# Kernel tuning notes

Measured on AMD Instinct MI355X. Metric: run time of the kernel, lower is better.

Reference implementation:

```python
import jax, jax.numpy as jnp
import numpy as np

EPS = 1e-12  # matches torch F.normalize default eps behavior for l2 norm

def l2norm(t):
    # normalize along last dim, like F.normalize(t, dim=-1)
    n = jnp.sqrt(jnp.sum(t * t, axis=-1, keepdims=True))
    return t / jnp.maximum(n, EPS)

def setup_inputs() -> dict:
    key = jax.random.key(0)
    k1, k2 = jax.random.split(key)
    x = jax.random.normal(k1, (4, 4096, 256), dtype=jnp.float32)
    embeddings = l2norm(jax.random.normal(k2, (8192, 256), dtype=jnp.float32))
    return {"x": x, "embeddings": embeddings}

def reference(x, embeddings):
    """Eval-mode forward of CosineSimilarityCodebook: returns (quantized, indices)."""
    shape = x.shape
    d = shape[-1]
    flatten = l2norm(x.reshape(-1, d))          # [N, d]
    emb_n = l2norm(embeddings)                  # [K, d]
    dist = flatten @ emb_n.T                    # [N, K] cosine similarity
    indices = jnp.argmax(dist, axis=-1)         # [N]
    indices = indices.reshape(shape[:-1])       # [...]
    quantized = embeddings[indices]             # gather from UN-normalized codebook
    return quantized, indices
```

## Files before the change

### kernel.cpp

```cpp
#include <hip/hip_runtime.h>
#include <stdint.h>


#define M_ROWS 16384
#define KCODES 8192
#define DDIM   256

#define BR   128
#define BCC  128
#define BK   32
#define NSPLIT 8
#define CPS  (KCODES / NSPLIT)
#define NSLICE ((CPS / BCC) * (DDIM / BK))
#define LSCALE     512.0f
#define INV_LSCALE (1.0f / 512.0f)
#define TILE_H 4096

typedef _Float16 half8v __attribute__((ext_vector_type(8)));
typedef float    f32x4  __attribute__((ext_vector_type(4)));

__device__ __forceinline__ unsigned int fkey(float f) {
    unsigned int u = __float_as_uint(f);
    return (u & 0x80000000u) ? ~u : (u | 0x80000000u);
}

__device__ __forceinline__ void gload16(const void* g, void* l) {
    __builtin_amdgcn_global_load_lds(
        (const __attribute__((address_space(1))) void*)g,
        (__attribute__((address_space(3))) void*)l, 16, 0, 0);
}


__global__ void norm_emb_kernel(const float* __restrict__ emb, float* __restrict__ inv_norm) {
    int row  = blockIdx.x * 4 + (threadIdx.x >> 6);
    int lane = threadIdx.x & 63;
    float4 v = reinterpret_cast<const float4*>(emb + row * DDIM)[lane];
    float s = v.x * v.x + v.y * v.y + v.z * v.z + v.w * v.w;
    #pragma unroll
    for (int m = 32; m; m >>= 1) s += __shfl_xor(s, m, 64);
    if (lane == 0) inv_norm[row] = 1.0f / fmaxf(sqrtf(s), 1e-12f);
}

__global__ void split_x_kernel(const float* __restrict__ x,
                               _Float16* __restrict__ xh, _Float16* __restrict__ xl) {
    int i = (blockIdx.x * 256 + threadIdx.x) * 8;
    float4 v0 = *reinterpret_cast<const float4*>(x + i);
    float4 v1 = *reinterpret_cast<const float4*>(x + i + 4);
    float v[8] = {v0.x, v0.y, v0.z, v0.w, v1.x, v1.y, v1.z, v1.w};
    half8v h, lo;
    #pragma unroll
    for (int j = 0; j < 8; ++j) {
        _Float16 hh = (_Float16)v[j];
        h[j]  = hh;
        lo[j] = (_Float16)((v[j] - (float)hh) * LSCALE);
    }
    *reinterpret_cast<half8v*>(xh + i) = h;
    *reinterpret_cast<half8v*>(xl + i) = lo;
}

__global__ void split_e_kernel(const float* __restrict__ emb, const float* __restrict__ invn,
                               _Float16* __restrict__ eh, _Float16* __restrict__ el) {
    int i = (blockIdx.x * 256 + threadIdx.x) * 8;
    float s = invn[i >> 8];
    float4 v0 = *reinterpret_cast<const float4*>(emb + i);
    float4 v1 = *reinterpret_cast<const float4*>(emb + i + 4);
    float v[8] = {v0.x * s, v0.y * s, v0.z * s, v0.w * s,
                  v1.x * s, v1.y * s, v1.z * s, v1.w * s};
    half8v h, lo;
    #pragma unroll
    for (int j = 0; j < 8; ++j) {
        _Float16 hh = (_Float16)v[j];
        h[j]  = hh;
        lo[j] = (_Float16)((v[j] - (float)hh) * LSCALE);
    }
    *reinterpret_cast<half8v*>(eh + i) = h;
    *reinterpret_cast<half8v*>(el + i) = lo;
}


__global__ __launch_bounds__(256, 2)
void mfma3_kernel(const _Float16* __restrict__ xh, const _Float16* __restrict__ xl,
                  const _Float16* __restrict__ eh, const _Float16* __restrict__ el,
                  unsigned long long* __restrict__ best) {
    __shared__ _Float16 lds[2][4 * TILE_H];

    const int t  = threadIdx.x;
    const int l  = t & 63;
    const int w  = t >> 6;
    const int wy = w >> 1, wx = w & 1;
    const int rb = blockIdx.x * BR;
    const int cs = blockIdx.y * CPS;
    const int lr = l & 15;
    const int kg = l >> 4;

    const int s_row = l >> 2;
    const int s_kg  = (l & 3) ^ ((l >> 3) & 3);

    const int rd_off = lr * 32 + (kg ^ ((lr >> 1) & 3)) * 8;
    const int a_base = wy * 64 * 32 + rd_off;
    const int b_base = wx * 64 * 32 + rd_off;

    const _Float16* gsrc = (w == 0) ? xh : (w == 1) ? xl : (w == 2) ? eh : el;
    const int g_is_x = (w < 2);

    float bestv[16];
    unsigned int bestc[16];
    #pragma unroll
    for (int i = 0; i < 16; ++i) { bestv[i] = -1e30f; bestc[i] = 0; }

    f32x4 acc[4][4];
    f32x4 acc2[4][4];

    {
        const _Float16* gp = gsrc + (g_is_x ? rb : cs) * DDIM + s_row * DDIM + s_kg * 8;
        _Float16* lp = &lds[0][w * TILE_H];
        #pragma unroll
        for (int c = 0; c < 8; ++c)
            gload16(gp + c * 16 * DDIM, lp + c * 512);
    }
    __syncthreads();

    int buf = 0;
    #pragma unroll 1
    for (int st = 0; st < NSLICE; ++st) {
        const int cb = cs + (st >> 3) * BCC;

        if ((st & 7) == 0) {
            #pragma unroll
            for (int m = 0; m < 4; ++m)
                #pragma unroll
                for (int n = 0; n < 4; ++n) {
                    acc[m][n]  = (f32x4){0.f, 0.f, 0.f, 0.f};
                    acc2[m][n] = (f32x4){0.f, 0.f, 0.f, 0.f};
                }
        }

        if (st + 1 < NSLICE) {
            const int ncb = cs + ((st + 1) >> 3) * BCC;
            const int ndb = ((st + 1) & 7) * BK;
            const _Float16* gp = gsrc + (g_is_x ? rb : ncb) * DDIM + ndb
                                 + s_row * DDIM + s_kg * 8;
            _Float16* lp = &lds[buf ^ 1][w * TILE_H];
            #pragma unroll
            for (int c = 0; c < 8; ++c)
                gload16(gp + c * 16 * DDIM, lp + c * 512);
        }

        const _Float16* L = lds[buf];
        half8v ah[4], al[4];
        #pragma unroll
        for (int m = 0; m < 4; ++m) {
            ah[m] = *reinterpret_cast<const half8v*>(&L[0 * TILE_H + a_base + m * 512]);
            al[m] = *reinterpret_cast<const half8v*>(&L[1 * TILE_H + a_base + m * 512]);
        }
        #pragma unroll
        for (int n = 0; n < 4; ++n) {
            half8v bh = *reinterpret_cast<const half8v*>(&L[2 * TILE_H + b_base + n * 512]);
            half8v bl = *reinterpret_cast<const half8v*>(&L[3 * TILE_H + b_base + n * 512]);
            #pragma unroll
            for (int m = 0; m < 4; ++m) {
                acc[m][n]  = __builtin_amdgcn_mfma_f32_16x16x32_f16(ah[m], bh, acc[m][n],  0, 0, 0);
                acc2[m][n] = __builtin_amdgcn_mfma_f32_16x16x32_f16(ah[m], bl, acc2[m][n], 0, 0, 0);
                acc2[m][n] = __builtin_amdgcn_mfma_f32_16x16x32_f16(al[m], bh, acc2[m][n], 0, 0, 0);
            }
        }

        if ((st & 7) == 7) {
            #pragma unroll
            for (int m = 0; m < 4; ++m)
                #pragma unroll
                for (int r = 0; r < 4; ++r) {
                    int bi = m * 4 + r;
                    #pragma unroll
                    for (int n = 0; n < 4; ++n) {
                        float v = acc[m][n][r] + acc2[m][n][r] * INV_LSCALE;
                        unsigned int code = cb + wx * 64 + n * 16 + lr;
                        if (v > bestv[bi]) { bestv[bi] = v; bestc[bi] = code; }
                    }
                }
        }

        __syncthreads();
        buf ^= 1;
    }

    #pragma unroll
    for (int mb = 1; mb < 16; mb <<= 1) {
        #pragma unroll
        for (int i = 0; i < 16; ++i) {
            float ov        = __shfl_xor(bestv[i], mb, 64);
            unsigned int oc = __shfl_xor(bestc[i], mb, 64);
            if (ov > bestv[i] || (ov == bestv[i] && oc < bestc[i])) {
                bestv[i] = ov; bestc[i] = oc;
            }
        }
    }
    if (lr == 0) {
        #pragma unroll
        for (int m = 0; m < 4; ++m)
            #pragma unroll
            for (int r = 0; r < 4; ++r) {
                int row_global = rb + wy * 64 + m * 16 + (l >> 4) * 4 + r;
                int bi = m * 4 + r;
                unsigned long long key =
                    ((unsigned long long)fkey(bestv[bi]) << 32) |
                    (unsigned long long)(0xFFFFFFFFu - bestc[bi]);
                atomicMax(&best[row_global], key);
            }
    }
}

#define LDP  (BK + 8)

typedef _Float16 half4v __attribute__((ext_vector_type(4)));

__device__ __forceinline__ void split4(float a, float b, float c, float d,
                                       half4v& h, half4v& lo) {
    h[0] = (_Float16)a; lo[0] = (_Float16)((a - (float)h[0]) * LSCALE);
    h[1] = (_Float16)b; lo[1] = (_Float16)((b - (float)h[1]) * LSCALE);
    h[2] = (_Float16)c; lo[2] = (_Float16)((c - (float)h[2]) * LSCALE);
    h[3] = (_Float16)d; lo[3] = (_Float16)((d - (float)h[3]) * LSCALE);
}

__global__ __launch_bounds__(256, 2)
void mfma_argmax_fb(const float* __restrict__ x, const float* __restrict__ emb,
                    const float* __restrict__ invn, unsigned long long* __restrict__ best) {
    __shared__ _Float16 Ah[BR][LDP];
    __shared__ _Float16 Al[BR][LDP];
    __shared__ _Float16 Bh[BCC][LDP];
    __shared__ _Float16 Bl[BCC][LDP];
    const int t = threadIdx.x, l = t & 63, wid = t >> 6;
    const int wy = wid >> 1, wx = wid & 1;
    const int rb = blockIdx.x * BR, cs = blockIdx.y * CPS;
    const int lr = l & 15, lk = (l >> 4) * 8;
    const int srow = t >> 3, sc4 = (t & 7) * 4;
    float bestv[16]; unsigned int bestc[16];
    #pragma unroll
    for (int i = 0; i < 16; ++i) { bestv[i] = -1e30f; bestc[i] = 0; }
    #pragma unroll 1
    for (int cc = 0; cc < CPS; cc += BCC) {
        const int cb = cs + cc;
        float bn[4];
        #pragma unroll
        for (int it = 0; it < 4; ++it) bn[it] = invn[cb + srow + it * 32];
        f32x4 acc[4][4], acc2[4][4];
        #pragma unroll
        for (int m = 0; m < 4; ++m)
            #pragma unroll
            for (int n = 0; n < 4; ++n) {
                acc[m][n] = (f32x4){0.f,0.f,0.f,0.f}; acc2[m][n] = (f32x4){0.f,0.f,0.f,0.f};
            }
        #pragma unroll 1
        for (int db = 0; db < DDIM; db += BK) {
            __syncthreads();
            #pragma unroll
            for (int it = 0; it < 4; ++it) {
                int row = srow + it * 32;
                float4 av = *reinterpret_cast<const float4*>(x + (size_t)(rb + row) * DDIM + db + sc4);
                half4v h, lo;
                split4(av.x, av.y, av.z, av.w, h, lo);
                *reinterpret_cast<half4v*>(&Ah[row][sc4]) = h;
                *reinterpret_cast<half4v*>(&Al[row][sc4]) = lo;
                float4 bv = *reinterpret_cast<const float4*>(emb + (size_t)(cb + row) * DDIM + db + sc4);
                float s = bn[it];
                split4(bv.x * s, bv.y * s, bv.z * s, bv.w * s, h, lo);
                *reinterpret_cast<half4v*>(&Bh[row][sc4]) = h;
                *reinterpret_cast<half4v*>(&Bl[row][sc4]) = lo;
            }
            __syncthreads();
            half8v ah[4], al[4];
            #pragma unroll
            for (int m = 0; m < 4; ++m) {
                ah[m] = *reinterpret_cast<const half8v*>(&Ah[wy * 64 + m * 16 + lr][lk]);
                al[m] = *reinterpret_cast<const half8v*>(&Al[wy * 64 + m * 16 + lr][lk]);
            }
            #pragma unroll
            for (int n = 0; n < 4; ++n) {
                half8v bh = *reinterpret_cast<const half8v*>(&Bh[wx * 64 + n * 16 + lr][lk]);
                half8v bl = *reinterpret_cast<const half8v*>(&Bl[wx * 64 + n * 16 + lr][lk]);
                #pragma unroll
                for (int m = 0; m < 4; ++m) {
                    acc[m][n]  = __builtin_amdgcn_mfma_f32_16x16x32_f16(ah[m], bh, acc[m][n],  0, 0, 0);
                    acc2[m][n] = __builtin_amdgcn_mfma_f32_16x16x32_f16(ah[m], bl, acc2[m][n], 0, 0, 0);
                    acc2[m][n] = __builtin_amdgcn_mfma_f32_16x16x32_f16(al[m], bh, acc2[m][n], 0, 0, 0);
                }
            }
        }
        #pragma unroll
        for (int m = 0; m < 4; ++m)
            #pragma unroll
            for (int r = 0; r < 4; ++r) {
                int bi = m * 4 + r;
                #pragma unroll
                for (int n = 0; n < 4; ++n) {
                    float v = acc[m][n][r] + acc2[m][n][r] * INV_LSCALE;
                    unsigned int code = cb + wx * 64 + n * 16 + lr;
                    if (v > bestv[bi]) { bestv[bi] = v; bestc[bi] = code; }
                }
            }
    }
    #pragma unroll
    for (int mb = 1; mb < 16; mb <<= 1) {
        #pragma unroll
        for (int i = 0; i < 16; ++i) {
            float ov = __shfl_xor(bestv[i], mb, 64);
            unsigned int oc = __shfl_xor(bestc[i], mb, 64);
            if (ov > bestv[i] || (ov == bestv[i] && oc < bestc[i])) { bestv[i] = ov; bestc[i] = oc; }
        }
    }
    if (lr == 0) {
        #pragma unroll
        for (int m = 0; m < 4; ++m)
            #pragma unroll
            for (int r = 0; r < 4; ++r) {
                int row_global = rb + wy * 64 + m * 16 + (l >> 4) * 4 + r;
                int bi = m * 4 + r;
                unsigned long long key = ((unsigned long long)fkey(bestv[bi]) << 32) |
                                         (unsigned long long)(0xFFFFFFFFu - bestc[bi]);
                atomicMax(&best[row_global], key);
            }
    }
}

__global__ void finalize_kernel(const unsigned long long* __restrict__ best,
                                const float* __restrict__ emb,
                                float* __restrict__ out) {
    int row = blockIdx.x;
    unsigned long long b = best[row];
    unsigned int code = 0xFFFFFFFFu - (unsigned int)(b & 0xFFFFFFFFull);
    out[(size_t)row * DDIM + threadIdx.x] = emb[(size_t)code * DDIM + threadIdx.x];
    if (threadIdx.x == 0) out[(size_t)M_ROWS * DDIM + row] = (float)code;
}

extern "C" void kernel_launch(void* const* d_in, const int* in_sizes, int n_in,
                              void* d_out, int out_size, void* d_ws, size_t ws_size,
                              hipStream_t stream) {
    const float* x   = (const float*)d_in[0];
    const float* emb = (const float*)d_in[1];
    float* out = (float*)d_out;

    unsigned long long* best = (unsigned long long*)d_ws;
    float* inv_norm = (float*)((char*)d_ws + 128 * 1024);
    const size_t split_off = 160 * 1024;
    const size_t need = split_off +
                        (size_t)M_ROWS * DDIM * 2 * sizeof(_Float16) +
                        (size_t)KCODES * DDIM * 2 * sizeof(_Float16);

    hipMemsetAsync(best, 0, M_ROWS * sizeof(unsigned long long), stream);
    norm_emb_kernel<<<KCODES / 4, 256, 0, stream>>>(emb, inv_norm);

    if (ws_size >= need) {
        _Float16* xh = (_Float16*)((char*)d_ws + split_off);
        _Float16* xl = xh + (size_t)M_ROWS * DDIM;
        _Float16* eh = xl + (size_t)M_ROWS * DDIM;
        _Float16* el = eh + (size_t)KCODES * DDIM;
        split_x_kernel<<<M_ROWS * DDIM / (256 * 8), 256, 0, stream>>>(x, xh, xl);
        split_e_kernel<<<KCODES * DDIM / (256 * 8), 256, 0, stream>>>(emb, inv_norm, eh, el);
        mfma3_kernel<<<dim3(M_ROWS / BR, NSPLIT), 256, 0, stream>>>(xh, xl, eh, el, best);
    } else {
        mfma_argmax_fb<<<dim3(M_ROWS / BR, NSPLIT), 256, 0, stream>>>(x, emb, inv_norm, best);
    }
    finalize_kernel<<<M_ROWS, 256, 0, stream>>>(best, emb, out);
}
```

Baseline: 289.9 us.

## Load A fragments directly from global, stage only codebook in LDS with 8 waves

```diff
diff --git a/kernel.cpp b/kernel.cpp
--- a/kernel.cpp
+++ b/kernel.cpp
@@ -14,8 +14,8 @@
 #define NSLICE ((CPS / BCC) * (DDIM / BK))
 #define LSCALE     512.0f
 #define INV_LSCALE (1.0f / 512.0f)
-#define TILE_H 4096
-
+
+typedef _Float16 half4v __attribute__((ext_vector_type(4)));
 typedef _Float16 half8v __attribute__((ext_vector_type(8)));
 typedef float    f32x4  __attribute__((ext_vector_type(4)));
 
@@ -31,10 +31,32 @@
 }
 
 
+__global__ void norm_split_e_kernel(const float* __restrict__ emb, float* __restrict__ inv_norm,
+                                    _Float16* __restrict__ eh, _Float16* __restrict__ el) {
+    int row  = blockIdx.x * 4 + (threadIdx.x >> 6);
+    int lane = threadIdx.x & 63;
+    float4 v = reinterpret_cast<const float4*>(emb + (size_t)row * DDIM)[lane];
+    float s = v.x * v.x + v.y * v.y + v.z * v.z + v.w * v.w;
+    #pragma unroll
+    for (int m = 32; m; m >>= 1) s += __shfl_xor(s, m, 64);
+    float inv = 1.0f / fmaxf(sqrtf(s), 1e-12f);
+    if (lane == 0) inv_norm[row] = inv;
+    float sv[4] = {v.x * inv, v.y * inv, v.z * inv, v.w * inv};
+    half4v h, lo;
+    #pragma unroll
+    for (int j = 0; j < 4; ++j) {
+        _Float16 hh = (_Float16)sv[j];
+        h[j]  = hh;
+        lo[j] = (_Float16)((sv[j] - (float)hh) * LSCALE);
+    }
+    *reinterpret_cast<half4v*>(eh + (size_t)row * DDIM + lane * 4) = h;
+    *reinterpret_cast<half4v*>(el + (size_t)row * DDIM + lane * 4) = lo;
+}
+
 __global__ void norm_emb_kernel(const float* __restrict__ emb, float* __restrict__ inv_norm) {
     int row  = blockIdx.x * 4 + (threadIdx.x >> 6);
     int lane = threadIdx.x & 63;
-    float4 v = reinterpret_cast<const float4*>(emb + row * DDIM)[lane];
+    float4 v = reinterpret_cast<const float4*>(emb + (size_t)row * DDIM)[lane];
     float s = v.x * v.x + v.y * v.y + v.z * v.z + v.w * v.w;
     #pragma unroll
     for (int m = 32; m; m >>= 1) s += __shfl_xor(s, m, 64);
@@ -58,65 +80,48 @@
     *reinterpret_cast<half8v*>(xl + i) = lo;
 }
 
-__global__ void split_e_kernel(const float* __restrict__ emb, const float* __restrict__ invn,
-                               _Float16* __restrict__ eh, _Float16* __restrict__ el) {
-    int i = (blockIdx.x * 256 + threadIdx.x) * 8;
-    float s = invn[i >> 8];
-    float4 v0 = *reinterpret_cast<const float4*>(emb + i);
-    float4 v1 = *reinterpret_cast<const float4*>(emb + i + 4);
-    float v[8] = {v0.x * s, v0.y * s, v0.z * s, v0.w * s,
-                  v1.x * s, v1.y * s, v1.z * s, v1.w * s};
-    half8v h, lo;
-    #pragma unroll
-    for (int j = 0; j < 8; ++j) {
-        _Float16 hh = (_Float16)v[j];
-        h[j]  = hh;
-        lo[j] = (_Float16)((v[j] - (float)hh) * LSCALE);
-    }
-    *reinterpret_cast<half8v*>(eh + i) = h;
-    *reinterpret_cast<half8v*>(el + i) = lo;
-}
-
-
-__global__ __launch_bounds__(256, 2)
-void mfma3_kernel(const _Float16* __restrict__ xh, const _Float16* __restrict__ xl,
-                  const _Float16* __restrict__ eh, const _Float16* __restrict__ el,
-                  unsigned long long* __restrict__ best) {
-    __shared__ _Float16 lds[2][4 * TILE_H];
+
+__global__ __launch_bounds__(512, 4)
+void mfma3g_kernel(const _Float16* __restrict__ xh, const _Float16* __restrict__ xl,
+                   const _Float16* __restrict__ eh, const _Float16* __restrict__ el,
+                   unsigned long long* __restrict__ best) {
+    __shared__ _Float16 lds[2][2][4096];
 
     const int t  = threadIdx.x;
     const int l  = t & 63;
     const int w  = t >> 6;
-    const int wy = w >> 1, wx = w & 1;
+    const int wy = w >> 1;
+    const int wx = w & 1;
     const int rb = blockIdx.x * BR;
     const int cs = blockIdx.y * CPS;
     const int lr = l & 15;
     const int kg = l >> 4;
 
-    const int s_row = l >> 2;
-    const int s_kg  = (l & 3) ^ ((l >> 3) & 3);
-
-    const int rd_off = lr * 32 + (kg ^ ((lr >> 1) & 3)) * 8;
-    const int a_base = wy * 64 * 32 + rd_off;
-    const int b_base = wx * 64 * 32 + rd_off;
-
-    const _Float16* gsrc = (w == 0) ? xh : (w == 1) ? xl : (w == 2) ? eh : el;
-    const int g_is_x = (w < 2);
-
-    float bestv[16];
-    unsigned int bestc[16];
-    #pragma unroll
-    for (int i = 0; i < 16; ++i) { bestv[i] = -1e30f; bestc[i] = 0; }
-
-    f32x4 acc[4][4];
-    f32x4 acc2[4][4];
+    const int s_code  = l >> 2;
+    const int s_kslot = (l & 3) ^ ((l >> 3) & 3);
+
+    const int b_off = (wx * 64 + lr) * 32 + (kg ^ ((lr >> 1) & 3)) * 8;
+
+    const size_t ar0 = (size_t)(rb + wy * 32 + lr) * DDIM + kg * 8;
+    const size_t ar1 = (size_t)(rb + wy * 32 + 16 + lr) * DDIM + kg * 8;
+    const _Float16* pah0 = xh + ar0;
+    const _Float16* pah1 = xh + ar1;
+    const _Float16* pal0 = xl + ar0;
+    const _Float16* pal1 = xl + ar1;
+
+    float bestv[8];
+    unsigned int bestc[8];
+    #pragma unroll
+    for (int i = 0; i < 8; ++i) { bestv[i] = -1e30f; bestc[i] = 0; }
+
+    f32x4 acc[2][4];
+    f32x4 acc2[2][4];
 
     {
-        const _Float16* gp = gsrc + (g_is_x ? rb : cs) * DDIM + s_row * DDIM + s_kg * 8;
-        _Float16* lp = &lds[0][w * TILE_H];
-        #pragma unroll
-        for (int c = 0; c < 8; ++c)
-            gload16(gp + c * 16 * DDIM, lp + c * 512);
+        const _Float16* gph = eh + (size_t)(cs + w * 16 + s_code) * DDIM + s_kslot * 8;
+        const _Float16* gpl = el + (size_t)(cs + w * 16 + s_code) * DDIM + s_kslot * 8;
+        gload16(gph, &lds[0][0][w * 512]);
+        gload16(gpl, &lds[0][1][w * 512]);
     }
     __syncthreads();
 
@@ -124,10 +129,11 @@
     #pragma unroll 1
     for (int st = 0; st < NSLICE; ++st) {
         const int cb = cs + (st >> 3) * BCC;
+        const int db = (st & 7) * BK;
 
         if ((st & 7) == 0) {
             #pragma unroll
-            for (int m = 0; m < 4; ++m)
+            for (int m = 0; m < 2; ++m)
                 #pragma unroll
                 for (int n = 0; n < 4; ++n) {
                     acc[m][n]  = (f32x4){0.f, 0.f, 0.f, 0.f};
@@ -138,36 +144,33 @@
         if (st + 1 < NSLICE) {
             const int ncb = cs + ((st + 1) >> 3) * BCC;
             const int ndb = ((st + 1) & 7) * BK;
-            const _Float16* gp = gsrc + (g_is_x ? rb : ncb) * DDIM + ndb
-                                 + s_row * DDIM + s_kg * 8;
-            _Float16* lp = &lds[buf ^ 1][w * TILE_H];
-            #pragma unroll
-            for (int c = 0; c < 8; ++c)
-                gload16(gp + c * 16 * DDIM, lp + c * 512);
-        }
-
-        const _Float16* L = lds[buf];
-        half8v ah[4], al[4];
-        #pragma unroll
-        for (int m = 0; m < 4; ++m) {
-            ah[m] = *reinterpret_cast<const half8v*>(&L[0 * TILE_H + a_base + m * 512]);
-            al[m] = *reinterpret_cast<const half8v*>(&L[1 * TILE_H + a_base + m * 512]);
-        }
+            const size_t so = (size_t)(ncb + w * 16 + s_code) * DDIM + ndb + s_kslot * 8;
+            gload16(eh + so, &lds[buf ^ 1][0][w * 512]);
+            gload16(el + so, &lds[buf ^ 1][1][w * 512]);
+        }
+
+        half8v ah0 = *reinterpret_cast<const half8v*>(pah0 + db);
+        half8v ah1 = *reinterpret_cast<const half8v*>(pah1 + db);
+        half8v al0 = *reinterpret_cast<const half8v*>(pal0 + db);
+        half8v al1 = *reinterpret_cast<const half8v*>(pal1 + db);
+
+        const _Float16* Lh = &lds[buf][0][0];
+        const _Float16* Ll = &lds[buf][1][0];
         #pragma unroll
         for (int n = 0; n < 4; ++n) {
-            half8v bh = *reinterpret_cast<const half8v*>(&L[2 * TILE_H + b_base + n * 512]);
-            half8v bl = *reinterpret_cast<const half8v*>(&L[3 * TILE_H + b_base + n * 512]);
-            #pragma unroll
-            for (int m = 0; m < 4; ++m) {
-                acc[m][n]  = __builtin_amdgcn_mfma_f32_16x16x32_f16(ah[m], bh, acc[m][n],  0, 0, 0);
-                acc2[m][n] = __builtin_amdgcn_mfma_f32_16x16x32_f16(ah[m], bl, acc2[m][n], 0, 0, 0);
-                acc2[m][n] = __builtin_amdgcn_mfma_f32_16x16x32_f16(al[m], bh, acc2[m][n], 0, 0, 0);
-            }
+            half8v bh = *reinterpret_cast<const half8v*>(Lh + b_off + n * 512);
+            half8v bl = *reinterpret_cast<const half8v*>(Ll + b_off + n * 512);
+            acc[0][n]  = __builtin_amdgcn_mfma_f32_16x16x32_f16(ah0, bh, acc[0][n],  0, 0, 0);
+            acc2[0][n] = __builtin_amdgcn_mfma_f32_16x16x32_f16(ah0, bl, acc2[0][n], 0, 0, 0);
+            acc2[0][n] = __builtin_amdgcn_mfma_f32_16x16x32_f16(al0, bh, acc2[0][n], 0, 0, 0);
+            acc[1][n]  = __builtin_amdgcn_mfma_f32_16x16x32_f16(ah1, bh, acc[1][n],  0, 0, 0);
+            acc2[1][n] = __builtin_amdgcn_mfma_f32_16x16x32_f16(ah1, bl, acc2[1][n], 0, 0, 0);
+            acc2[1][n] = __builtin_amdgcn_mfma_f32_16x16x32_f16(al1, bh, acc2[1][n], 0, 0, 0);
         }
 
         if ((st & 7) == 7) {
             #pragma unroll
-            for (int m = 0; m < 4; ++m)
+            for (int m = 0; m < 2; ++m)
                 #pragma unroll
                 for (int r = 0; r < 4; ++r) {
                     int bi = m * 4 + r;
@@ -187,7 +190,7 @@
     #pragma unroll
     for (int mb = 1; mb < 16; mb <<= 1) {
         #pragma unroll
-        for (int i = 0; i < 16; ++i) {
+        for (int i = 0; i < 8; ++i) {
             float ov        = __shfl_xor(bestv[i], mb, 64);
             unsigned int oc = __shfl_xor(bestc[i], mb, 64);
             if (ov > bestv[i] || (ov == bestv[i] && oc < bestc[i])) {
@@ -197,10 +200,10 @@
     }
     if (lr == 0) {
         #pragma unroll
-        for (int m = 0; m < 4; ++m)
+        for (int m = 0; m < 2; ++m)
             #pragma unroll
             for (int r = 0; r < 4; ++r) {
-                int row_global = rb + wy * 64 + m * 16 + (l >> 4) * 4 + r;
+                int row_global = rb + wy * 32 + m * 16 + (l >> 4) * 4 + r;
                 int bi = m * 4 + r;
                 unsigned long long key =
                     ((unsigned long long)fkey(bestv[bi]) << 32) |
@@ -211,8 +214,6 @@
 }
 
 #define LDP  (BK + 8)
-
-typedef _Float16 half4v __attribute__((ext_vector_type(4)));
 
 __device__ __forceinline__ void split4(float a, float b, float c, float d,
                                        half4v& h, half4v& lo) {
@@ -325,11 +326,13 @@
 __global__ void finalize_kernel(const unsigned long long* __restrict__ best,
                                 const float* __restrict__ emb,
                                 float* __restrict__ out) {
-    int row = blockIdx.x;
+    int row  = blockIdx.x * 4 + (threadIdx.x >> 6);
+    int lane = threadIdx.x & 63;
     unsigned long long b = best[row];
     unsigned int code = 0xFFFFFFFFu - (unsigned int)(b & 0xFFFFFFFFull);
-    out[(size_t)row * DDIM + threadIdx.x] = emb[(size_t)code * DDIM + threadIdx.x];
-    if (threadIdx.x == 0) out[(size_t)M_ROWS * DDIM + row] = (float)code;
+    float4 v = reinterpret_cast<const float4*>(emb + (size_t)code * DDIM)[lane];
+    reinterpret_cast<float4*>(out + (size_t)row * DDIM)[lane] = v;
+    if (lane == 0) out[(size_t)M_ROWS * DDIM + row] = (float)code;
 }
 
 extern "C" void kernel_launch(void* const* d_in, const int* in_sizes, int n_in,
@@ -347,18 +350,18 @@
                         (size_t)KCODES * DDIM * 2 * sizeof(_Float16);
 
     hipMemsetAsync(best, 0, M_ROWS * sizeof(unsigned long long), stream);
-    norm_emb_kernel<<<KCODES / 4, 256, 0, stream>>>(emb, inv_norm);
 
     if (ws_size >= need) {
         _Float16* xh = (_Float16*)((char*)d_ws + split_off);
         _Float16* xl = xh + (size_t)M_ROWS * DDIM;
         _Float16* eh = xl + (size_t)M_ROWS * DDIM;
         _Float16* el = eh + (size_t)KCODES * DDIM;
+        norm_split_e_kernel<<<KCODES / 4, 256, 0, stream>>>(emb, inv_norm, eh, el);
         split_x_kernel<<<M_ROWS * DDIM / (256 * 8), 256, 0, stream>>>(x, xh, xl);
-        split_e_kernel<<<KCODES * DDIM / (256 * 8), 256, 0, stream>>>(emb, inv_norm, eh, el);
-        mfma3_kernel<<<dim3(M_ROWS / BR, NSPLIT), 256, 0, stream>>>(xh, xl, eh, el, best);
+        mfma3g_kernel<<<dim3(M_ROWS / BR, NSPLIT), 512, 0, stream>>>(xh, xl, eh, el, best);
     } else {
+        norm_emb_kernel<<<KCODES / 4, 256, 0, stream>>>(emb, inv_norm);
         mfma_argmax_fb<<<dim3(M_ROWS / BR, NSPLIT), 256, 0, stream>>>(x, emb, inv_norm, best);
     }
-    finalize_kernel<<<M_ROWS, 256, 0, stream>>>(best, emb, out);
-}
+    finalize_kernel<<<M_ROWS / 4, 256, 0, stream>>>(best, emb, out);
+}
```

Result: slower. 362.7 us (+25.1%).

## Fuse emb norm with split, pipeline LDS loads with vmcnt waits, vectorize finalize

Applied to the files above, without the earlier changes.

```diff
diff --git a/kernel.cpp b/kernel.cpp
--- a/kernel.cpp
+++ b/kernel.cpp
@@ -16,6 +16,7 @@
 #define INV_LSCALE (1.0f / 512.0f)
 #define TILE_H 4096
 
+typedef _Float16 half4v __attribute__((ext_vector_type(4)));
 typedef _Float16 half8v __attribute__((ext_vector_type(8)));
 typedef float    f32x4  __attribute__((ext_vector_type(4)));
 
@@ -31,10 +32,32 @@
 }
 
 
+__global__ void norm_split_e_kernel(const float* __restrict__ emb, float* __restrict__ inv_norm,
+                                    _Float16* __restrict__ eh, _Float16* __restrict__ el) {
+    int row  = blockIdx.x * 4 + (threadIdx.x >> 6);
+    int lane = threadIdx.x & 63;
+    float4 v = reinterpret_cast<const float4*>(emb + (size_t)row * DDIM)[lane];
+    float s = v.x * v.x + v.y * v.y + v.z * v.z + v.w * v.w;
+    #pragma unroll
+    for (int m = 32; m; m >>= 1) s += __shfl_xor(s, m, 64);
+    float inv = 1.0f / fmaxf(sqrtf(s), 1e-12f);
+    if (lane == 0) inv_norm[row] = inv;
+    float sv[4] = {v.x * inv, v.y * inv, v.z * inv, v.w * inv};
+    half4v h, lo;
+    #pragma unroll
+    for (int j = 0; j < 4; ++j) {
+        _Float16 hh = (_Float16)sv[j];
+        h[j]  = hh;
+        lo[j] = (_Float16)((sv[j] - (float)hh) * LSCALE);
+    }
+    *reinterpret_cast<half4v*>(eh + (size_t)row * DDIM + lane * 4) = h;
+    *reinterpret_cast<half4v*>(el + (size_t)row * DDIM + lane * 4) = lo;
+}
+
 __global__ void norm_emb_kernel(const float* __restrict__ emb, float* __restrict__ inv_norm) {
     int row  = blockIdx.x * 4 + (threadIdx.x >> 6);
     int lane = threadIdx.x & 63;
-    float4 v = reinterpret_cast<const float4*>(emb + row * DDIM)[lane];
+    float4 v = reinterpret_cast<const float4*>(emb + (size_t)row * DDIM)[lane];
     float s = v.x * v.x + v.y * v.y + v.z * v.z + v.w * v.w;
     #pragma unroll
     for (int m = 32; m; m >>= 1) s += __shfl_xor(s, m, 64);
@@ -58,30 +81,11 @@
     *reinterpret_cast<half8v*>(xl + i) = lo;
 }
 
-__global__ void split_e_kernel(const float* __restrict__ emb, const float* __restrict__ invn,
-                               _Float16* __restrict__ eh, _Float16* __restrict__ el) {
-    int i = (blockIdx.x * 256 + threadIdx.x) * 8;
-    float s = invn[i >> 8];
-    float4 v0 = *reinterpret_cast<const float4*>(emb + i);
-    float4 v1 = *reinterpret_cast<const float4*>(emb + i + 4);
-    float v[8] = {v0.x * s, v0.y * s, v0.z * s, v0.w * s,
-                  v1.x * s, v1.y * s, v1.z * s, v1.w * s};
-    half8v h, lo;
-    #pragma unroll
-    for (int j = 0; j < 8; ++j) {
-        _Float16 hh = (_Float16)v[j];
-        h[j]  = hh;
-        lo[j] = (_Float16)((v[j] - (float)hh) * LSCALE);
-    }
-    *reinterpret_cast<half8v*>(eh + i) = h;
-    *reinterpret_cast<half8v*>(el + i) = lo;
-}
-
 
 __global__ __launch_bounds__(256, 2)
-void mfma3_kernel(const _Float16* __restrict__ xh, const _Float16* __restrict__ xl,
-                  const _Float16* __restrict__ eh, const _Float16* __restrict__ el,
-                  unsigned long long* __restrict__ best) {
+void mfma3p_kernel(const _Float16* __restrict__ xh, const _Float16* __restrict__ xl,
+                   const _Float16* __restrict__ eh, const _Float16* __restrict__ el,
+                   unsigned long long* __restrict__ best) {
     __shared__ _Float16 lds[2][4 * TILE_H];
 
     const int t  = threadIdx.x;
@@ -118,7 +122,6 @@
         for (int c = 0; c < 8; ++c)
             gload16(gp + c * 16 * DDIM, lp + c * 512);
     }
-    __syncthreads();
 
     int buf = 0;
     #pragma unroll 1
@@ -144,7 +147,12 @@
             #pragma unroll
             for (int c = 0; c < 8; ++c)
                 gload16(gp + c * 16 * DDIM, lp + c * 512);
-        }
+            asm volatile("s_waitcnt vmcnt(8)" ::: "memory");
+        } else {
+            asm volatile("s_waitcnt vmcnt(0)" ::: "memory");
+        }
+        __builtin_amdgcn_s_barrier();
+        __builtin_amdgcn_sched_barrier(0);
 
         const _Float16* L = lds[buf];
         half8v ah[4], al[4];
@@ -153,6 +161,7 @@
             ah[m] = *reinterpret_cast<const half8v*>(&L[0 * TILE_H + a_base + m * 512]);
             al[m] = *reinterpret_cast<const half8v*>(&L[1 * TILE_H + a_base + m * 512]);
         }
+        __builtin_amdgcn_s_setprio(1);
         #pragma unroll
         for (int n = 0; n < 4; ++n) {
             half8v bh = *reinterpret_cast<const half8v*>(&L[2 * TILE_H + b_base + n * 512]);
@@ -164,6 +173,7 @@
                 acc2[m][n] = __builtin_amdgcn_mfma_f32_16x16x32_f16(al[m], bh, acc2[m][n], 0, 0, 0);
             }
         }
+        __builtin_amdgcn_s_setprio(0);
 
         if ((st & 7) == 7) {
             #pragma unroll
@@ -180,7 +190,8 @@
                 }
         }
 
-        __syncthreads();
+        __builtin_amdgcn_sched_barrier(0);
+        __builtin_amdgcn_s_barrier();
         buf ^= 1;
     }
 
@@ -211,8 +222,6 @@
 }
 
 #define LDP  (BK + 8)
-
-typedef _Float16 half4v __attribute__((ext_vector_type(4)));
 
 __device__ __forceinline__ void split4(float a, float b, float c, float d,
                                        half4v& h, half4v& lo) {
@@ -325,11 +334,13 @@
 __global__ void finalize_kernel(const unsigned long long* __restrict__ best,
                                 const float* __restrict__ emb,
                                 float* __restrict__ out) {
-    int row = blockIdx.x;
+    int row  = blockIdx.x * 4 + (threadIdx.x >> 6);
+    int lane = threadIdx.x & 63;
     unsigned long long b = best[row];
     unsigned int code = 0xFFFFFFFFu - (unsigned int)(b & 0xFFFFFFFFull);
-    out[(size_t)row * DDIM + threadIdx.x] = emb[(size_t)code * DDIM + threadIdx.x];
-    if (threadIdx.x == 0) out[(size_t)M_ROWS * DDIM + row] = (float)code;
+    float4 v = reinterpret_cast<const float4*>(emb + (size_t)code * DDIM)[lane];
+    reinterpret_cast<float4*>(out + (size_t)row * DDIM)[lane] = v;
+    if (lane == 0) out[(size_t)M_ROWS * DDIM + row] = (float)code;
 }
 
 extern "C" void kernel_launch(void* const* d_in, const int* in_sizes, int n_in,
@@ -347,18 +358,18 @@
                         (size_t)KCODES * DDIM * 2 * sizeof(_Float16);
 
     hipMemsetAsync(best, 0, M_ROWS * sizeof(unsigned long long), stream);
-    norm_emb_kernel<<<KCODES / 4, 256, 0, stream>>>(emb, inv_norm);
 
     if (ws_size >= need) {
         _Float16* xh = (_Float16*)((char*)d_ws + split_off);
         _Float16* xl = xh + (size_t)M_ROWS * DDIM;
         _Float16* eh = xl + (size_t)M_ROWS * DDIM;
         _Float16* el = eh + (size_t)KCODES * DDIM;
+        norm_split_e_kernel<<<KCODES / 4, 256, 0, stream>>>(emb, inv_norm, eh, el);
         split_x_kernel<<<M_ROWS * DDIM / (256 * 8), 256, 0, stream>>>(x, xh, xl);
-        split_e_kernel<<<KCODES * DDIM / (256 * 8), 256, 0, stream>>>(emb, inv_norm, eh, el);
-        mfma3_kernel<<<dim3(M_ROWS / BR, NSPLIT), 256, 0, stream>>>(xh, xl, eh, el, best);
+        mfma3p_kernel<<<dim3(M_ROWS / BR, NSPLIT), 256, 0, stream>>>(xh, xl, eh, el, best);
     } else {
+        norm_emb_kernel<<<KCODES / 4, 256, 0, stream>>>(emb, inv_norm);
         mfma_argmax_fb<<<dim3(M_ROWS / BR, NSPLIT), 256, 0, stream>>>(x, emb, inv_norm, best);
     }
-    finalize_kernel<<<M_ROWS, 256, 0, stream>>>(best, emb, out);
-}
+    finalize_kernel<<<M_ROWS / 4, 256, 0, stream>>>(best, emb, out);
+}
```

After: 285.3 us. About the same (-1.6%).
